# Optimization experiments

Hardware: AMD Instinct MI355X
Metric: run time of the kernel (lower is better)

The kernel has to match this reference:

```python
import jax, jax.numpy as jnp
import numpy as np

# DCNv2 (ModulatedDeformConvPack) config, matching init_kwargs
STRIDE, PAD, DIL = 1, 1, 1
DG = 8            # deformable_groups
KH = KW = 3
CIN, COUT = 64, 64
B, H, W = 2, 128, 128


def setup_inputs() -> dict:
    key = jax.random.key(0)
    k1, k2, k3, k4 = jax.random.split(key, 4)
    x = jax.random.normal(k1, (B, CIN, H, W), dtype=jnp.float32)
    # conv_offset: Conv2d(CIN, DG*3*KH*KW, 3, stride=1, pad=1). Zero-init in the
    # original; use small random weights so offsets/mask are non-trivial.
    conv_offset_w = jax.random.normal(k2, (DG * 3 * KH * KW, CIN, KH, KW), dtype=jnp.float32) * 0.01
    conv_offset_b = jax.random.normal(k3, (DG * 3 * KH * KW,), dtype=jnp.float32) * 0.01
    n = CIN * KH * KW
    stdv = 1.0 / np.sqrt(n)
    weight = jax.random.uniform(k4, (COUT, CIN, KH, KW), dtype=jnp.float32, minval=-stdv, maxval=stdv)
    bias = jnp.zeros((COUT,), dtype=jnp.float32)
    return {"x": x, "conv_offset_w": conv_offset_w, "conv_offset_b": conv_offset_b,
            "weight": weight, "bias": bias}


def _dcn_v2(x, conv_offset_w, conv_offset_b, weight, bias):
    Bn, Cin, Hh, Ww = x.shape
    Cout, _, kh, kw = weight.shape
    K = kh * kw
    cpg = Cin // DG  # channels per deformable group

    # offset/mask predictor conv (standard conv)
    out = jax.lax.conv_general_dilated(
        x, conv_offset_w, window_strides=(STRIDE, STRIDE),
        padding=[(PAD, PAD), (PAD, PAD)], rhs_dilation=(DIL, DIL),
        dimension_numbers=("NCHW", "OIHW", "NCHW")) + conv_offset_b[None, :, None, None]
    o1, o2, mask = jnp.split(out, 3, axis=1)
    offset = jnp.concatenate([o1, o2], axis=1)          # (B, 2*DG*K, Ho, Wo)
    Ho, Wo = offset.shape[2], offset.shape[3]
    # CUDA kernel reads offset channels as [dg, K, (y, x)]
    off = offset.reshape(Bn, DG, K, 2, Ho, Wo)
    off_y = off[:, :, :, 0]                              # (B, DG, K, Ho, Wo)
    off_x = off[:, :, :, 1]
    mask = jax.nn.sigmoid(mask).reshape(Bn, DG, K, Ho, Wo)

    ki = (jnp.arange(K) // kw).astype(x.dtype)           # tap row index
    kj = (jnp.arange(K) % kw).astype(x.dtype)            # tap col index
    base_y = jnp.arange(Ho, dtype=x.dtype) * STRIDE - PAD
    base_x = jnp.arange(Wo, dtype=x.dtype) * STRIDE - PAD
    py = off_y + base_y[None, None, None, :, None] + (ki * DIL)[None, None, :, None, None]
    px = off_x + base_x[None, None, None, None, :] + (kj * DIL)[None, None, :, None, None]

    y0 = jnp.floor(py)
    x0 = jnp.floor(px)
    ly = py - y0
    lx = px - x0
    y0i = y0.astype(jnp.int32)
    x0i = x0.astype(jnp.int32)

    xg = x.reshape(Bn, DG, cpg, Hh, Ww)
    bi = jnp.arange(Bn)[:, None, None, None, None]
    gi = jnp.arange(DG)[None, :, None, None, None]

    def gather(yi, xi):
        # zero padding outside the image (matches CUDA corner validity checks)
        valid = (yi >= 0) & (yi <= Hh - 1) & (xi >= 0) & (xi <= Ww - 1)
        yc = jnp.clip(yi, 0, Hh - 1)
        xc = jnp.clip(xi, 0, Ww - 1)
        v = xg[bi, gi, :, yc, xc]                        # (B, DG, K, Ho, Wo, cpg)
        return v * valid[..., None].astype(x.dtype)

    v00 = gather(y0i, x0i)
    v01 = gather(y0i, x0i + 1)
    v10 = gather(y0i + 1, x0i)
    v11 = gather(y0i + 1, x0i + 1)
    hy, hx = 1.0 - ly, 1.0 - lx
    val = ((hy * hx)[..., None] * v00 + (hy * lx)[..., None] * v01 +
           (ly * hx)[..., None] * v10 + (ly * lx)[..., None] * v11)

    col = val * mask[..., None]                          # modulated columns
    wr = weight.reshape(Cout, DG, cpg, K)
    y = jnp.einsum('bgkhwc,ogck->bohw', col, wr) + bias[None, :, None, None]
    return y


def reference(x, conv_offset_w, conv_offset_b, weight, bias):
    return _dcn_v2(x, conv_offset_w, conv_offset_b, weight, bias)
```

## Files before the change

### kernel.cpp

```cpp
#include <hip/hip_runtime.h>
#include <hip/hip_fp16.h>

constexpr int BB = 2;
constexpr int CINc = 64;
constexpr int HWc = 128 * 128;
constexpr int OCOFFc = 216;
constexpr int XP = 130;

constexpr size_t XT_BYTES  = (size_t)BB * 8 * XP * XP * 8 * 2;
constexpr size_t WB1_OFF   = XT_BYTES;
constexpr size_t WB1_BYTES = (size_t)9 * 8 * 256 * 8 * 2;
constexpr size_t WM_OFF    = WB1_OFF + WB1_BYTES;
constexpr size_t WM_BYTES  = (size_t)8 * 12 * 64 * 8 * 2;
constexpr size_t WS_NEEDED = WM_OFF + WM_BYTES;

typedef _Float16 f16x8 __attribute__((ext_vector_type(8)));
typedef float    f32x4 __attribute__((ext_vector_type(4)));

__global__ void prep_all(const float* __restrict__ x, const float* __restrict__ w_off,
                         const float* __restrict__ weight,
                         __half* __restrict__ xT, __half* __restrict__ wB1,
                         __half* __restrict__ wM) {
    int bid = blockIdx.x;
    if (bid < 1024) {
        int site = bid * 256 + threadIdx.x;
        int pix = site & (HWc - 1);
        int bdg = site >> 14;
        int dg = bdg & 7, b = bdg >> 3;
        int y = pix >> 7, xc = pix & 127;
        const float* xp = x + (size_t)(b * CINc + dg * 8) * HWc + pix;
        __half2 h0 = __halves2half2(__float2half(xp[0 * HWc]), __float2half(xp[1 * HWc]));
        __half2 h1 = __halves2half2(__float2half(xp[2 * HWc]), __float2half(xp[3 * HWc]));
        __half2 h2 = __halves2half2(__float2half(xp[4 * HWc]), __float2half(xp[5 * HWc]));
        __half2 h3 = __halves2half2(__float2half(xp[6 * HWc]), __float2half(xp[7 * HWc]));
        __half2* o = reinterpret_cast<__half2*>(
            xT + (((size_t)(b * 8 + dg) * XP + y + 1) * XP + xc + 1) * 8);
        o[0] = h0; o[1] = h1; o[2] = h2; o[3] = h3;
        return;
    }
    int idx = (bid - 1024) * 256 + threadIdx.x;
    if (idx < 9 * 8 * 256 * 8) {
        int ci = idx & 7;
        int oc = (idx >> 3) & 255;
        int c  = (idx >> 11) & 7;
        int tap = idx >> 14;
        float v = (oc < OCOFFc) ? w_off[oc * 576 + (c * 8 + ci) * 9 + tap] : 0.f;
        wB1[idx] = __float2half(v);
    } else if (idx < 9 * 8 * 256 * 8 + 8 * 12 * 64 * 8) {
        int j = idx - 9 * 8 * 256 * 8;
        int c = j & 7;
        int oc = (j >> 3) & 63;
        int tg = j >> 9;
        int tap = tg % 12;
        int dg = tg / 12;
        float v = (tap < 9) ? weight[oc * 576 + (dg * 8 + c) * 9 + tap] : 0.f;
        wM[j] = __float2half(v);
    } else {
        int j2 = idx - (9 * 8 * 256 * 8 + 8 * 12 * 64 * 8);
        if (j2 < 16 * 516) {
            int plane = j2 / 516;
            int p = j2 - plane * 516;
            int y, xx;
            if (p < 130)      { y = 0;           xx = p; }
            else if (p < 260) { y = 129;         xx = p - 130; }
            else if (p < 388) { y = 1 + p - 260; xx = 0; }
            else              { y = 1 + p - 388; xx = 129; }
            uint4 z = {0u, 0u, 0u, 0u};
            *reinterpret_cast<uint4*>(xT + (((size_t)plane * XP + y) * XP + xx) * 8) = z;
        }
    }
}

#define DCN_ISSUE(DG, G, W)                                                    \
  {                                                                            \
    const int dg_ = (DG);                                                      \
    const __half* xb_ = xT + (size_t)(b * 8 + dg_) * XP * XP * 8;              \
    _Pragma("unroll")                                                          \
    for (int s_ = 0; s_ < 3; ++s_) {                                           \
      const int kg_ = s_ * 4 + lh;                                             \
      if (kg_ < 9) {                                                           \
        const int r3_ = (dg_ * 9 + kg_) * 3;                                   \
        float oy_ = __half2float(offsb[r3_ * 132 + px]);                       \
        float ox_ = __half2float(offsb[(r3_ + 1) * 132 + px]);                 \
        float mk_ = __half2float(offsb[(r3_ + 2) * 132 + px]);                 \
        const int ki_ = kg_ / 3, kj_ = kg_ - ki_ * 3;                          \
        float sy_ = oy_ + (float)(gy - 1 + ki_);                               \
        float sx_ = ox_ + (float)(gx - 1 + kj_);                               \
        float y0f_ = floorf(sy_), x0f_ = floorf(sx_);                          \
        int iy0_ = (int)y0f_, ix0_ = (int)x0f_;                                \
        float ly_ = sy_ - y0f_, lx_ = sx_ - x0f_;                              \
        float hy_ = 1.f - ly_, hx_ = 1.f - lx_;                                \
        float vy0_ = ((unsigned)iy0_ < 128u) ? 1.f : 0.f;                      \
        float vy1_ = ((unsigned)(iy0_ + 1) < 128u) ? 1.f : 0.f;                \
        float vx0_ = ((unsigned)ix0_ < 128u) ? 1.f : 0.f;                      \
        float vx1_ = ((unsigned)(ix0_ + 1) < 128u) ? 1.f : 0.f;                \
        W[s_ * 4 + 0] = hy_ * hx_ * vy0_ * vx0_ * mk_;                         \
        W[s_ * 4 + 1] = hy_ * lx_ * vy0_ * vx1_ * mk_;                         \
        W[s_ * 4 + 2] = ly_ * hx_ * vy1_ * vx0_ * mk_;                         \
        W[s_ * 4 + 3] = ly_ * lx_ * vy1_ * vx1_ * mk_;                         \
        int y0c_ = min(max(iy0_, 0), 127), y1c_ = min(max(iy0_ + 1, 0), 127);  \
        int x0c_ = min(max(ix0_, 0), 127), x1c_ = min(max(ix0_ + 1, 0), 127);  \
        G[s_ * 4 + 0] = *reinterpret_cast<const float4*>(xb_ + ((size_t)(y0c_ + 1) * XP + x0c_ + 1) * 8); \
        G[s_ * 4 + 1] = *reinterpret_cast<const float4*>(xb_ + ((size_t)(y0c_ + 1) * XP + x1c_ + 1) * 8); \
        G[s_ * 4 + 2] = *reinterpret_cast<const float4*>(xb_ + ((size_t)(y1c_ + 1) * XP + x0c_ + 1) * 8); \
        G[s_ * 4 + 3] = *reinterpret_cast<const float4*>(xb_ + ((size_t)(y1c_ + 1) * XP + x1c_ + 1) * 8); \
      } else {                                                                 \
        const float4 z4_ = {0.f, 0.f, 0.f, 0.f};                               \
        W[s_ * 4 + 0] = 0.f; W[s_ * 4 + 1] = 0.f;                              \
        W[s_ * 4 + 2] = 0.f; W[s_ * 4 + 3] = 0.f;                              \
        G[s_ * 4 + 0] = z4_; G[s_ * 4 + 1] = z4_;                              \
        G[s_ * 4 + 2] = z4_; G[s_ * 4 + 3] = z4_;                              \
      }                                                                        \
    }                                                                          \
  }

#define DCN_CONSUME(DG, G, W)                                                  \
  {                                                                            \
    const int dg_ = (DG);                                                      \
    f16x8 bf_[12];                                                             \
    _Pragma("unroll")                                                          \
    for (int s_ = 0; s_ < 3; ++s_)                                             \
      _Pragma("unroll")                                                        \
      for (int n_ = 0; n_ < 4; ++n_)                                           \
        bf_[s_ * 4 + n_] = *reinterpret_cast<const f16x8*>(                    \
            wM + (size_t)((dg_ * 12 + s_ * 4 + lh) * 64 + n_ * 16 + l15) * 8); \
    f16x8 af_[3];                                                              \
    _Pragma("unroll")                                                          \
    for (int s_ = 0; s_ < 3; ++s_) {                                           \
      __half2 W00_ = __float2half2_rn(W[s_ * 4 + 0]);                          \
      __half2 W01_ = __float2half2_rn(W[s_ * 4 + 1]);                          \
      __half2 W10_ = __float2half2_rn(W[s_ * 4 + 2]);                          \
      __half2 W11_ = __float2half2_rn(W[s_ * 4 + 3]);                          \
      const __half2* a00_ = reinterpret_cast<const __half2*>(&G[s_ * 4 + 0]);  \
      const __half2* a01_ = reinterpret_cast<const __half2*>(&G[s_ * 4 + 1]);  \
      const __half2* a10_ = reinterpret_cast<const __half2*>(&G[s_ * 4 + 2]);  \
      const __half2* a11_ = reinterpret_cast<const __half2*>(&G[s_ * 4 + 3]);  \
      __align__(16) __half2 rr_[4];                                            \
      _Pragma("unroll")                                                        \
      for (int cc_ = 0; cc_ < 4; ++cc_)                                        \
        rr_[cc_] = __hfma2(a00_[cc_], W00_,                                    \
                   __hfma2(a01_[cc_], W01_,                                    \
                   __hfma2(a10_[cc_], W10_, __hmul2(a11_[cc_], W11_))));       \
      af_[s_] = *reinterpret_cast<const f16x8*>(rr_);                          \
    }                                                                          \
    _Pragma("unroll")                                                          \
    for (int s_ = 0; s_ < 3; ++s_)                                             \
      _Pragma("unroll")                                                        \
      for (int n_ = 0; n_ < 4; ++n_)                                           \
        acc2[n_] = __builtin_amdgcn_mfma_f32_16x16x32_f16(                     \
            af_[s_], bf_[s_ * 4 + n_], acc2[n_], 0, 0, 0);                     \
  }

__global__ __launch_bounds__(512, 2) void dcn_fused_k(
        const __half* __restrict__ xT, const __half* __restrict__ wB1,
        const float* __restrict__ cob, const __half* __restrict__ wM,
        const float* __restrict__ bias, float* __restrict__ out) {
    __shared__ __half xs[1440 * 8];
    __shared__ __half offsb[216 * 132];
    const int tid = threadIdx.x;
    const int fid = blockIdx.x + (blockIdx.y << 3) + (blockIdx.z << 7);
    const int vid = ((fid & 7) << 5) + (fid >> 3);
    const int bx = vid & 7;
    const int by = (vid >> 3) & 15;
    const int b  = vid >> 7;

    #pragma unroll
    for (int it = 0; it < 3; ++it) {
        int idx = tid + it * 512;
        if (idx < 1440) {
            int yl = idx / 144;
            int rem = idx - yl * 144;
            int cl = rem >> 3, sl = rem & 7;
            int dg = sl ^ (cl & 7);
            float4 v = *reinterpret_cast<const float4*>(
                xT + (((size_t)(b * 8 + dg) * XP + by * 8 + yl) * XP + bx * 16 + cl) * 8);
            *reinterpret_cast<float4*>(xs + idx * 8) = v;
        }
    }
    __syncthreads();

    const int lane = tid & 63;
    const int wid = tid >> 6;
    const int l15 = lane & 15, lh = lane >> 4;

    {
        const int wr = wid & 1;
        const int wc = wid >> 1;
        f32x4 acc[4][4];
        const f32x4 zero = {0.f, 0.f, 0.f, 0.f};
        #pragma unroll
        for (int ty = 0; ty < 4; ++ty)
            #pragma unroll
            for (int ot = 0; ot < 4; ++ot) acc[ty][ot] = zero;

        #pragma unroll 3
        for (int tap = 0; tap < 9; ++tap) {
            const int r = tap / 3, s = tap - r * 3;
            const int j = l15 + s;
            #pragma unroll
            for (int h = 0; h < 2; ++h) {
                const int c = h * 4 + lh;
                const int sl = c ^ (j & 7);
                f16x8 af[4], bf[4];
                #pragma unroll
                for (int ot = 0; ot < 4; ++ot) {
                    int oc = wc * 64 + ot * 16 + l15;
                    bf[ot] = *reinterpret_cast<const f16x8*>(
                        wB1 + (size_t)(((tap * 8 + c) * 256 + oc)) * 8);
                }
                #pragma unroll
                for (int ty = 0; ty < 4; ++ty) {
                    int row = wr * 4 + ty + r;
                    af[ty] = *reinterpret_cast<const f16x8*>(xs + (row * 18 + j) * 64 + sl * 8);
                }
                #pragma unroll
                for (int ty = 0; ty < 4; ++ty)
                    #pragma unroll
                    for (int ot = 0; ot < 4; ++ot)
                        acc[ty][ot] = __builtin_amdgcn_mfma_f32_16x16x32_f16(
                            af[ty], bf[ot], acc[ty][ot], 0, 0, 0);
            }
        }

        #pragma unroll
        for (int ot = 0; ot < 4; ++ot) {
            int oc = wc * 64 + ot * 16 + l15;
            if (oc < OCOFFc) {
                float bi = cob[oc];
                bool sig = (oc >= 144);
                int dg, k, comp;
                if (oc < 144) { dg = oc / 18; int rem = oc - dg * 18; k = rem >> 1; comp = rem & 1; }
                else          { int mm = oc - 144; dg = mm / 9; k = mm - dg * 9; comp = 2; }
                int r3 = (dg * 9 + k) * 3 + comp;
                #pragma unroll
                for (int ty = 0; ty < 4; ++ty) {
                    int px = (wr * 4 + ty) * 16 + lh * 4;
                    float v0 = acc[ty][ot][0] + bi, v1 = acc[ty][ot][1] + bi;
                    float v2 = acc[ty][ot][2] + bi, v3 = acc[ty][ot][3] + bi;
                    if (sig) {
                        v0 = 1.f / (1.f + __expf(-v0)); v1 = 1.f / (1.f + __expf(-v1));
                        v2 = 1.f / (1.f + __expf(-v2)); v3 = 1.f / (1.f + __expf(-v3));
                    }
                    __half2* d = reinterpret_cast<__half2*>(&offsb[r3 * 132 + px]);
                    d[0] = __halves2half2(__float2half(v0), __float2half(v1));
                    d[1] = __halves2half2(__float2half(v2), __float2half(v3));
                }
            }
        }
    }
    __syncthreads();

    const int px = wid * 16 + l15;
    const int gy = by * 8 + wid;
    const int gx = bx * 16 + l15;

    f32x4 acc2[4];
    const f32x4 zero2 = {0.f, 0.f, 0.f, 0.f};
    #pragma unroll
    for (int n = 0; n < 4; ++n) acc2[n] = zero2;

    float4 gA[12]; float wA[12];
    float4 gB[12]; float wB[12];

    DCN_ISSUE(0, gA, wA);
    #pragma unroll 1
    for (int d = 0; d < 8; d += 2) {
        DCN_ISSUE(d + 1, gB, wB);
        DCN_CONSUME(d, gA, wA);
        if (d + 2 < 8) DCN_ISSUE(d + 2, gA, wA);
        DCN_CONSUME(d + 1, gB, wB);
    }

    #pragma unroll
    for (int n = 0; n < 4; ++n) {
        int oc = n * 16 + l15;
        float bi = bias[oc];
        float4 v = make_float4(acc2[n][0] + bi, acc2[n][1] + bi,
                               acc2[n][2] + bi, acc2[n][3] + bi);
        *reinterpret_cast<float4*>(
            out + (size_t)(b * 64 + oc) * HWc + gy * 128 + bx * 16 + lh * 4) = v;
    }
}

extern "C" void kernel_launch(void* const* d_in, const int* in_sizes, int n_in,
                              void* d_out, int out_size, void* d_ws, size_t ws_size,
                              hipStream_t stream) {
    const float* x      = (const float*)d_in[0];
    const float* w_off  = (const float*)d_in[1];
    const float* cob    = (const float*)d_in[2];
    const float* weight = (const float*)d_in[3];
    const float* bias   = (const float*)d_in[4];
    float* out = (float*)d_out;
    if (ws_size < WS_NEEDED) return;

    char* ws = (char*)d_ws;
    __half* xT  = (__half*)ws;
    __half* wB1 = (__half*)(ws + WB1_OFF);
    __half* wM  = (__half*)(ws + WM_OFF);

    prep_all<<<1825, 256, 0, stream>>>(x, w_off, weight, xT, wB1, wM);
    dcn_fused_k<<<dim3(8, 16, 2), 512, 0, stream>>>(xT, wB1, cob, wM, bias, out);
}
```

Baseline: 39.36 us.

## Halve fused DCN tile to 8x8 pixels and split output channels across waves

Each block of the fused kernel now covers an 8x8 pixel tile instead of 8x16, which doubles the grid to 512 blocks and halves the shared-memory footprint for the input halo and offset buffer. The offset-conv MFMA tiling is remapped so each wave covers 32 pixels, and the deformable stage splits the 64 output channels between wave halves, with each wave handling 16 pixels and 32 channels. The goal is to raise occupancy and CU coverage on a small problem. The cost is that bilinear sampling and weight computation are now done twice per pixel (once per channel half), and the halo overhead per pixel is higher.

```diff
diff --git a/kernel.cpp b/kernel.cpp
--- a/kernel.cpp
+++ b/kernel.cpp
@@ -80,9 +80,9 @@
       const int kg_ = s_ * 4 + lh;                                             \
       if (kg_ < 9) {                                                           \
         const int r3_ = (dg_ * 9 + kg_) * 3;                                   \
-        float oy_ = __half2float(offsb[r3_ * 132 + px]);                       \
-        float ox_ = __half2float(offsb[(r3_ + 1) * 132 + px]);                 \
-        float mk_ = __half2float(offsb[(r3_ + 2) * 132 + px]);                 \
+        float oy_ = __half2float(offsb[r3_ * 66 + px]);                        \
+        float ox_ = __half2float(offsb[(r3_ + 1) * 66 + px]);                  \
+        float mk_ = __half2float(offsb[(r3_ + 2) * 66 + px]);                  \
         const int ki_ = kg_ / 3, kj_ = kg_ - ki_ * 3;                          \
         float sy_ = oy_ + (float)(gy - 1 + ki_);                               \
         float sx_ = ox_ + (float)(gx - 1 + kj_);                               \
@@ -117,13 +117,13 @@
 #define DCN_CONSUME(DG, G, W)                                                  \
   {                                                                            \
     const int dg_ = (DG);                                                      \
-    f16x8 bf_[12];                                                             \
+    f16x8 bf_[6];                                                              \
     _Pragma("unroll")                                                          \
     for (int s_ = 0; s_ < 3; ++s_)                                             \
       _Pragma("unroll")                                                        \
-      for (int n_ = 0; n_ < 4; ++n_)                                           \
-        bf_[s_ * 4 + n_] = *reinterpret_cast<const f16x8*>(                    \
-            wM + (size_t)((dg_ * 12 + s_ * 4 + lh) * 64 + n_ * 16 + l15) * 8); \
+      for (int n_ = 0; n_ < 2; ++n_)                                           \
+        bf_[s_ * 2 + n_] = *reinterpret_cast<const f16x8*>(                    \
+            wM + (size_t)((dg_ * 12 + s_ * 4 + lh) * 64 + nh * 32 + n_ * 16 + l15) * 8); \
     f16x8 af_[3];                                                              \
     _Pragma("unroll")                                                          \
     for (int s_ = 0; s_ < 3; ++s_) {                                           \
@@ -146,34 +146,34 @@
     _Pragma("unroll")                                                          \
     for (int s_ = 0; s_ < 3; ++s_)                                             \
       _Pragma("unroll")                                                        \
-      for (int n_ = 0; n_ < 4; ++n_)                                           \
+      for (int n_ = 0; n_ < 2; ++n_)                                           \
         acc2[n_] = __builtin_amdgcn_mfma_f32_16x16x32_f16(                     \
-            af_[s_], bf_[s_ * 4 + n_], acc2[n_], 0, 0, 0);                     \
+            af_[s_], bf_[s_ * 2 + n_], acc2[n_], 0, 0, 0);                     \
   }
 
 __global__ __launch_bounds__(512, 2) void dcn_fused_k(
         const __half* __restrict__ xT, const __half* __restrict__ wB1,
         const float* __restrict__ cob, const __half* __restrict__ wM,
         const float* __restrict__ bias, float* __restrict__ out) {
-    __shared__ __half xs[1440 * 8];
-    __shared__ __half offsb[216 * 132];
+    __shared__ __half xs[800 * 8];
+    __shared__ __half offsb[216 * 66];
     const int tid = threadIdx.x;
-    const int fid = blockIdx.x + (blockIdx.y << 3) + (blockIdx.z << 7);
-    const int vid = ((fid & 7) << 5) + (fid >> 3);
-    const int bx = vid & 7;
-    const int by = (vid >> 3) & 15;
-    const int b  = vid >> 7;
+    const int fid = blockIdx.x + (blockIdx.y << 4) + (blockIdx.z << 8);
+    const int vid = ((fid & 7) << 6) + (fid >> 3);
+    const int bx = vid & 15;
+    const int by = (vid >> 4) & 15;
+    const int b  = vid >> 8;
 
     #pragma unroll
-    for (int it = 0; it < 3; ++it) {
+    for (int it = 0; it < 2; ++it) {
         int idx = tid + it * 512;
-        if (idx < 1440) {
-            int yl = idx / 144;
-            int rem = idx - yl * 144;
+        if (idx < 800) {
+            int yl = idx / 80;
+            int rem = idx - yl * 80;
             int cl = rem >> 3, sl = rem & 7;
             int dg = sl ^ (cl & 7);
             float4 v = *reinterpret_cast<const float4*>(
-                xT + (((size_t)(b * 8 + dg) * XP + by * 8 + yl) * XP + bx * 16 + cl) * 8);
+                xT + (((size_t)(b * 8 + dg) * XP + by * 8 + yl) * XP + bx * 8 + cl) * 8);
             *reinterpret_cast<float4*>(xs + idx * 8) = v;
         }
     }
@@ -184,47 +184,47 @@
     const int l15 = lane & 15, lh = lane >> 4;
 
     {
-        const int wr = wid & 1;
-        const int wc = wid >> 1;
-        f32x4 acc[4][4];
+        const int wm = wid & 1;
+        const int wn = wid >> 1;
+        f32x4 acc[2][4];
         const f32x4 zero = {0.f, 0.f, 0.f, 0.f};
         #pragma unroll
-        for (int ty = 0; ty < 4; ++ty)
+        for (int f = 0; f < 2; ++f)
             #pragma unroll
-            for (int ot = 0; ot < 4; ++ot) acc[ty][ot] = zero;
+            for (int ot = 0; ot < 4; ++ot) acc[f][ot] = zero;
 
         #pragma unroll 3
         for (int tap = 0; tap < 9; ++tap) {
             const int r = tap / 3, s = tap - r * 3;
-            const int j = l15 + s;
+            const int j = (l15 & 7) + s;
             #pragma unroll
             for (int h = 0; h < 2; ++h) {
                 const int c = h * 4 + lh;
                 const int sl = c ^ (j & 7);
-                f16x8 af[4], bf[4];
+                f16x8 af[2], bf[4];
                 #pragma unroll
                 for (int ot = 0; ot < 4; ++ot) {
-                    int oc = wc * 64 + ot * 16 + l15;
+                    int oc = wn * 64 + ot * 16 + l15;
                     bf[ot] = *reinterpret_cast<const f16x8*>(
                         wB1 + (size_t)(((tap * 8 + c) * 256 + oc)) * 8);
                 }
                 #pragma unroll
-                for (int ty = 0; ty < 4; ++ty) {
-                    int row = wr * 4 + ty + r;
-                    af[ty] = *reinterpret_cast<const f16x8*>(xs + (row * 18 + j) * 64 + sl * 8);
+                for (int f = 0; f < 2; ++f) {
+                    int row = wm * 4 + f * 2 + (l15 >> 3) + r;
+                    af[f] = *reinterpret_cast<const f16x8*>(xs + (row * 10 + j) * 64 + sl * 8);
                 }
                 #pragma unroll
-                for (int ty = 0; ty < 4; ++ty)
+                for (int f = 0; f < 2; ++f)
                     #pragma unroll
                     for (int ot = 0; ot < 4; ++ot)
-                        acc[ty][ot] = __builtin_amdgcn_mfma_f32_16x16x32_f16(
-                            af[ty], bf[ot], acc[ty][ot], 0, 0, 0);
+                        acc[f][ot] = __builtin_amdgcn_mfma_f32_16x16x32_f16(
+                            af[f], bf[ot], acc[f][ot], 0, 0, 0);
             }
         }
 
         #pragma unroll
         for (int ot = 0; ot < 4; ++ot) {
-            int oc = wc * 64 + ot * 16 + l15;
+            int oc = wn * 64 + ot * 16 + l15;
             if (oc < OCOFFc) {
                 float bi = cob[oc];
                 bool sig = (oc >= 144);
@@ -233,15 +233,15 @@
                 else          { int mm = oc - 144; dg = mm / 9; k = mm - dg * 9; comp = 2; }
                 int r3 = (dg * 9 + k) * 3 + comp;
                 #pragma unroll
-                for (int ty = 0; ty < 4; ++ty) {
-                    int px = (wr * 4 + ty) * 16 + lh * 4;
-                    float v0 = acc[ty][ot][0] + bi, v1 = acc[ty][ot][1] + bi;
-                    float v2 = acc[ty][ot][2] + bi, v3 = acc[ty][ot][3] + bi;
+                for (int f = 0; f < 2; ++f) {
+                    int px = wm * 32 + f * 16 + lh * 4;
+                    float v0 = acc[f][ot][0] + bi, v1 = acc[f][ot][1] + bi;
+                    float v2 = acc[f][ot][2] + bi, v3 = acc[f][ot][3] + bi;
                     if (sig) {
                         v0 = 1.f / (1.f + __expf(-v0)); v1 = 1.f / (1.f + __expf(-v1));
                         v2 = 1.f / (1.f + __expf(-v2)); v3 = 1.f / (1.f + __expf(-v3));
                     }
-                    __half2* d = reinterpret_cast<__half2*>(&offsb[r3 * 132 + px]);
+                    __half2* d = reinterpret_cast<__half2*>(&offsb[r3 * 66 + px]);
                     d[0] = __halves2half2(__float2half(v0), __float2half(v1));
                     d[1] = __halves2half2(__float2half(v2), __float2half(v3));
                 }
@@ -250,14 +250,14 @@
     }
     __syncthreads();
 
-    const int px = wid * 16 + l15;
-    const int gy = by * 8 + wid;
-    const int gx = bx * 16 + l15;
-
-    f32x4 acc2[4];
+    const int m  = wid & 3;
+    const int nh = wid >> 2;
+    const int px = m * 16 + l15;
+    const int gy = by * 8 + (px >> 3), gx = bx * 8 + (px & 7);
+
+    f32x4 acc2[2];
     const f32x4 zero2 = {0.f, 0.f, 0.f, 0.f};
-    #pragma unroll
-    for (int n = 0; n < 4; ++n) acc2[n] = zero2;
+    acc2[0] = zero2; acc2[1] = zero2;
 
     float4 gA[12]; float wA[12];
     float4 gB[12]; float wB[12];
@@ -271,14 +271,16 @@
         DCN_CONSUME(d + 1, gB, wB);
     }
 
+    const int gyo = by * 8 + m * 2 + (lh >> 1);
+    const int gx0 = bx * 8 + (lh & 1) * 4;
     #pragma unroll
-    for (int n = 0; n < 4; ++n) {
-        int oc = n * 16 + l15;
+    for (int n = 0; n < 2; ++n) {
+        int oc = nh * 32 + n * 16 + l15;
         float bi = bias[oc];
         float4 v = make_float4(acc2[n][0] + bi, acc2[n][1] + bi,
                                acc2[n][2] + bi, acc2[n][3] + bi);
         *reinterpret_cast<float4*>(
-            out + (size_t)(b * 64 + oc) * HWc + gy * 128 + bx * 16 + lh * 4) = v;
+            out + (size_t)(b * 64 + oc) * HWc + gyo * 128 + gx0) = v;
     }
 }
 
@@ -299,5 +301,5 @@
     __half* wM  = (__half*)(ws + WM_OFF);
 
     prep_all<<<1825, 256, 0, stream>>>(x, w_off, weight, xT, wB1, wM);
-    dcn_fused_k<<<dim3(8, 16, 2), 512, 0, stream>>>(xT, wB1, cob, wM, bias, out);
+    dcn_fused_k<<<dim3(16, 16, 2), 512, 0, stream>>>(xT, wB1, cob, wM, bias, out);
 }
```

Result: slower. 49.65 us (+26.1%).

## Software-pipeline weight fragment loads and raise MFMA priority in fused DCN kernel

Applied to the files above, without the earlier changes.

Weight B-fragments for both the offset conv and the deformable MFMA stage are now prefetched one step ahead into double buffers, so global loads overlap the preceding MFMA batch. MFMA sections are wrapped in s_setprio to favour matrix issue, bilinear weights are packed as half2 to save registers, and the offset LDS row pitch shrinks from 132 to 130. Launch bounds drop from 2 to 1 block per CU, giving more registers for the extra buffers at the cost of occupancy.

```diff
diff --git a/kernel.cpp b/kernel.cpp
--- a/kernel.cpp
+++ b/kernel.cpp
@@ -71,6 +71,17 @@
     }
 }
 
+#define DCN_LOADBF(DG, BF)                                                     \
+  {                                                                            \
+    const int dgb_ = (DG);                                                     \
+    _Pragma("unroll")                                                          \
+    for (int s_ = 0; s_ < 3; ++s_)                                             \
+      _Pragma("unroll")                                                        \
+      for (int n_ = 0; n_ < 4; ++n_)                                           \
+        BF[s_ * 4 + n_] = *reinterpret_cast<const f16x8*>(                     \
+            wM + (size_t)((dgb_ * 12 + s_ * 4 + lh) * 64 + n_ * 16 + l15) * 8);\
+  }
+
 #define DCN_ISSUE(DG, G, W)                                                    \
   {                                                                            \
     const int dg_ = (DG);                                                      \
@@ -80,9 +91,9 @@
       const int kg_ = s_ * 4 + lh;                                             \
       if (kg_ < 9) {                                                           \
         const int r3_ = (dg_ * 9 + kg_) * 3;                                   \
-        float oy_ = __half2float(offsb[r3_ * 132 + px]);                       \
-        float ox_ = __half2float(offsb[(r3_ + 1) * 132 + px]);                 \
-        float mk_ = __half2float(offsb[(r3_ + 2) * 132 + px]);                 \
+        float oy_ = __half2float(offsb[r3_ * 130 + px]);                       \
+        float ox_ = __half2float(offsb[(r3_ + 1) * 130 + px]);                 \
+        float mk_ = __half2float(offsb[(r3_ + 2) * 130 + px]);                 \
         const int ki_ = kg_ / 3, kj_ = kg_ - ki_ * 3;                          \
         float sy_ = oy_ + (float)(gy - 1 + ki_);                               \
         float sx_ = ox_ + (float)(gx - 1 + kj_);                               \
@@ -94,10 +105,10 @@
         float vy1_ = ((unsigned)(iy0_ + 1) < 128u) ? 1.f : 0.f;                \
         float vx0_ = ((unsigned)ix0_ < 128u) ? 1.f : 0.f;                      \
         float vx1_ = ((unsigned)(ix0_ + 1) < 128u) ? 1.f : 0.f;                \
-        W[s_ * 4 + 0] = hy_ * hx_ * vy0_ * vx0_ * mk_;                         \
-        W[s_ * 4 + 1] = hy_ * lx_ * vy0_ * vx1_ * mk_;                         \
-        W[s_ * 4 + 2] = ly_ * hx_ * vy1_ * vx0_ * mk_;                         \
-        W[s_ * 4 + 3] = ly_ * lx_ * vy1_ * vx1_ * mk_;                         \
+        W[s_ * 2 + 0] = __floats2half2_rn(hy_ * hx_ * vy0_ * vx0_ * mk_,      \
+                                          hy_ * lx_ * vy0_ * vx1_ * mk_);      \
+        W[s_ * 2 + 1] = __floats2half2_rn(ly_ * hx_ * vy1_ * vx0_ * mk_,      \
+                                          ly_ * lx_ * vy1_ * vx1_ * mk_);      \
         int y0c_ = min(max(iy0_, 0), 127), y1c_ = min(max(iy0_ + 1, 0), 127);  \
         int x0c_ = min(max(ix0_, 0), 127), x1c_ = min(max(ix0_ + 1, 0), 127);  \
         G[s_ * 4 + 0] = *reinterpret_cast<const float4*>(xb_ + ((size_t)(y0c_ + 1) * XP + x0c_ + 1) * 8); \
@@ -106,31 +117,23 @@
         G[s_ * 4 + 3] = *reinterpret_cast<const float4*>(xb_ + ((size_t)(y1c_ + 1) * XP + x1c_ + 1) * 8); \
       } else {                                                                 \
         const float4 z4_ = {0.f, 0.f, 0.f, 0.f};                               \
-        W[s_ * 4 + 0] = 0.f; W[s_ * 4 + 1] = 0.f;                              \
-        W[s_ * 4 + 2] = 0.f; W[s_ * 4 + 3] = 0.f;                              \
+        W[s_ * 2 + 0] = __float2half2_rn(0.f);                                 \
+        W[s_ * 2 + 1] = __float2half2_rn(0.f);                                 \
         G[s_ * 4 + 0] = z4_; G[s_ * 4 + 1] = z4_;                              \
         G[s_ * 4 + 2] = z4_; G[s_ * 4 + 3] = z4_;                              \
       }                                                                        \
     }                                                                          \
   }
 
-#define DCN_CONSUME(DG, G, W)                                                  \
+#define DCN_CONSUME(DG, G, W, BF)                                              \
   {                                                                            \
-    const int dg_ = (DG);                                                      \
-    f16x8 bf_[12];                                                             \
-    _Pragma("unroll")                                                          \
-    for (int s_ = 0; s_ < 3; ++s_)                                             \
-      _Pragma("unroll")                                                        \
-      for (int n_ = 0; n_ < 4; ++n_)                                           \
-        bf_[s_ * 4 + n_] = *reinterpret_cast<const f16x8*>(                    \
-            wM + (size_t)((dg_ * 12 + s_ * 4 + lh) * 64 + n_ * 16 + l15) * 8); \
     f16x8 af_[3];                                                              \
     _Pragma("unroll")                                                          \
     for (int s_ = 0; s_ < 3; ++s_) {                                           \
-      __half2 W00_ = __float2half2_rn(W[s_ * 4 + 0]);                          \
-      __half2 W01_ = __float2half2_rn(W[s_ * 4 + 1]);                          \
-      __half2 W10_ = __float2half2_rn(W[s_ * 4 + 2]);                          \
-      __half2 W11_ = __float2half2_rn(W[s_ * 4 + 3]);                          \
+      __half2 W00_ = __half2half2(__low2half(W[s_ * 2 + 0]));                  \
+      __half2 W01_ = __half2half2(__high2half(W[s_ * 2 + 0]));                 \
+      __half2 W10_ = __half2half2(__low2half(W[s_ * 2 + 1]));                  \
+      __half2 W11_ = __half2half2(__high2half(W[s_ * 2 + 1]));                 \
       const __half2* a00_ = reinterpret_cast<const __half2*>(&G[s_ * 4 + 0]);  \
       const __half2* a01_ = reinterpret_cast<const __half2*>(&G[s_ * 4 + 1]);  \
       const __half2* a10_ = reinterpret_cast<const __half2*>(&G[s_ * 4 + 2]);  \
@@ -143,20 +146,22 @@
                    __hfma2(a10_[cc_], W10_, __hmul2(a11_[cc_], W11_))));       \
       af_[s_] = *reinterpret_cast<const f16x8*>(rr_);                          \
     }                                                                          \
+    __builtin_amdgcn_s_setprio(1);                                             \
     _Pragma("unroll")                                                          \
     for (int s_ = 0; s_ < 3; ++s_)                                             \
       _Pragma("unroll")                                                        \
       for (int n_ = 0; n_ < 4; ++n_)                                           \
         acc2[n_] = __builtin_amdgcn_mfma_f32_16x16x32_f16(                     \
-            af_[s_], bf_[s_ * 4 + n_], acc2[n_], 0, 0, 0);                     \
+            af_[s_], BF[s_ * 4 + n_], acc2[n_], 0, 0, 0);                      \
+    __builtin_amdgcn_s_setprio(0);                                             \
   }
 
-__global__ __launch_bounds__(512, 2) void dcn_fused_k(
+__global__ __launch_bounds__(512, 1) void dcn_fused_k(
         const __half* __restrict__ xT, const __half* __restrict__ wB1,
         const float* __restrict__ cob, const __half* __restrict__ wM,
         const float* __restrict__ bias, float* __restrict__ out) {
     __shared__ __half xs[1440 * 8];
-    __shared__ __half offsb[216 * 132];
+    __shared__ __half offsb[216 * 130];
     const int tid = threadIdx.x;
     const int fid = blockIdx.x + (blockIdx.y << 3) + (blockIdx.z << 7);
     const int vid = ((fid & 7) << 5) + (fid >> 3);
@@ -186,6 +191,7 @@
     {
         const int wr = wid & 1;
         const int wc = wid >> 1;
+        const int ocb = wc * 64 + l15;
         f32x4 acc[4][4];
         const f32x4 zero = {0.f, 0.f, 0.f, 0.f};
         #pragma unroll
@@ -193,32 +199,58 @@
             #pragma unroll
             for (int ot = 0; ot < 4; ++ot) acc[ty][ot] = zero;
 
-        #pragma unroll 3
+        f16x8 bfA[4], bfB[4];
+        #pragma unroll
+        for (int ot = 0; ot < 4; ++ot)
+            bfA[ot] = *reinterpret_cast<const f16x8*>(
+                wB1 + (size_t)(lh * 256 + ocb + ot * 16) * 8);
+
+        #pragma unroll 1
         for (int tap = 0; tap < 9; ++tap) {
             const int r = tap / 3, s = tap - r * 3;
             const int j = l15 + s;
             #pragma unroll
-            for (int h = 0; h < 2; ++h) {
-                const int c = h * 4 + lh;
-                const int sl = c ^ (j & 7);
-                f16x8 af[4], bf[4];
-                #pragma unroll
-                for (int ot = 0; ot < 4; ++ot) {
-                    int oc = wc * 64 + ot * 16 + l15;
-                    bf[ot] = *reinterpret_cast<const f16x8*>(
-                        wB1 + (size_t)(((tap * 8 + c) * 256 + oc)) * 8);
-                }
-                #pragma unroll
-                for (int ty = 0; ty < 4; ++ty) {
-                    int row = wr * 4 + ty + r;
-                    af[ty] = *reinterpret_cast<const f16x8*>(xs + (row * 18 + j) * 64 + sl * 8);
-                }
+            for (int ot = 0; ot < 4; ++ot)
+                bfB[ot] = *reinterpret_cast<const f16x8*>(
+                    wB1 + (size_t)((tap * 8 + 4 + lh) * 256 + ocb + ot * 16) * 8);
+            {
+                const int sl = lh ^ (j & 7);
+                f16x8 af[4];
+                #pragma unroll
+                for (int ty = 0; ty < 4; ++ty)
+                    af[ty] = *reinterpret_cast<const f16x8*>(
+                        xs + ((wr * 4 + ty + r) * 18 + j) * 64 + sl * 8);
+                __builtin_amdgcn_s_setprio(1);
                 #pragma unroll
                 for (int ty = 0; ty < 4; ++ty)
                     #pragma unroll
                     for (int ot = 0; ot < 4; ++ot)
                         acc[ty][ot] = __builtin_amdgcn_mfma_f32_16x16x32_f16(
-                            af[ty], bf[ot], acc[ty][ot], 0, 0, 0);
+                            af[ty], bfA[ot], acc[ty][ot], 0, 0, 0);
+                __builtin_amdgcn_s_setprio(0);
+            }
+            if (tap < 8) {
+                #pragma unroll
+                for (int ot = 0; ot < 4; ++ot)
+                    bfA[ot] = *reinterpret_cast<const f16x8*>(
+                        wB1 + (size_t)(((tap + 1) * 8 + lh) * 256 + ocb + ot * 16) * 8);
+            }
+            {
+                const int c = 4 + lh;
+                const int sl = c ^ (j & 7);
+                f16x8 af[4];
+                #pragma unroll
+                for (int ty = 0; ty < 4; ++ty)
+                    af[ty] = *reinterpret_cast<const f16x8*>(
+                        xs + ((wr * 4 + ty + r) * 18 + j) * 64 + sl * 8);
+                __builtin_amdgcn_s_setprio(1);
+                #pragma unroll
+                for (int ty = 0; ty < 4; ++ty)
+                    #pragma unroll
+                    for (int ot = 0; ot < 4; ++ot)
+                        acc[ty][ot] = __builtin_amdgcn_mfma_f32_16x16x32_f16(
+                            af[ty], bfB[ot], acc[ty][ot], 0, 0, 0);
+                __builtin_amdgcn_s_setprio(0);
             }
         }
 
@@ -241,7 +273,7 @@
                         v0 = 1.f / (1.f + __expf(-v0)); v1 = 1.f / (1.f + __expf(-v1));
                         v2 = 1.f / (1.f + __expf(-v2)); v3 = 1.f / (1.f + __expf(-v3));
                     }
-                    __half2* d = reinterpret_cast<__half2*>(&offsb[r3 * 132 + px]);
+                    __half2* d = reinterpret_cast<__half2*>(&offsb[r3 * 130 + px]);
                     d[0] = __halves2half2(__float2half(v0), __float2half(v1));
                     d[1] = __halves2half2(__float2half(v2), __float2half(v3));
                 }
@@ -259,16 +291,22 @@
     #pragma unroll
     for (int n = 0; n < 4; ++n) acc2[n] = zero2;
 
-    float4 gA[12]; float wA[12];
-    float4 gB[12]; float wB[12];
-
-    DCN_ISSUE(0, gA, wA);
+    float4 gX[12], gY[12];
+    __half2 wX[6], wY[6];
+    f16x8 bfX[12], bfY[12];
+
+    DCN_LOADBF(0, bfX);
+    DCN_ISSUE(0, gX, wX);
     #pragma unroll 1
     for (int d = 0; d < 8; d += 2) {
-        DCN_ISSUE(d + 1, gB, wB);
-        DCN_CONSUME(d, gA, wA);
-        if (d + 2 < 8) DCN_ISSUE(d + 2, gA, wA);
-        DCN_CONSUME(d + 1, gB, wB);
+        DCN_LOADBF(d + 1, bfY);
+        DCN_ISSUE(d + 1, gY, wY);
+        DCN_CONSUME(d, gX, wX, bfX);
+        if (d < 6) {
+            DCN_LOADBF(d + 2, bfX);
+            DCN_ISSUE(d + 2, gX, wX);
+        }
+        DCN_CONSUME(d + 1, gY, wY, bfY);
     }
 
     #pragma unroll
```

Result: slower. 58.64 us (+49.0%).

## Pipeline deformable sampling per tap-slice with fp16 weights and repacked offset layout

Applied to the files above, without the earlier changes.

Splits each deformable group's gather-and-MFMA work into three tap slices and double-buffers at slice granularity rather than per full group. Per-slice weight fragments are loaded alongside the gathers, and the bilinear weights are stored as packed half2. The shared offset/mask buffer is reorganized pixel-major so each thread fetches offset-y, offset-x and mask with one 8-byte load. The aim is lower register pressure and finer overlap of gather latency with MFMA, at the cost of scattered 2-byte shared stores in the offset epilogue and possible bank conflicts from the stride-36 layout.

```diff
diff --git a/kernel.cpp b/kernel.cpp
--- a/kernel.cpp
+++ b/kernel.cpp
@@ -71,18 +71,23 @@
     }
 }
 
-#define DCN_ISSUE(DG, G, W)                                                    \
+#define DCN_IC(D_, S_, BF, G, W, ACT)                                          \
   {                                                                            \
-    const int dg_ = (DG);                                                      \
-    const __half* xb_ = xT + (size_t)(b * 8 + dg_) * XP * XP * 8;              \
-    _Pragma("unroll")                                                          \
-    for (int s_ = 0; s_ < 3; ++s_) {                                           \
-      const int kg_ = s_ * 4 + lh;                                             \
-      if (kg_ < 9) {                                                           \
-        const int r3_ = (dg_ * 9 + kg_) * 3;                                   \
-        float oy_ = __half2float(offsb[r3_ * 132 + px]);                       \
-        float ox_ = __half2float(offsb[(r3_ + 1) * 132 + px]);                 \
-        float mk_ = __half2float(offsb[(r3_ + 2) * 132 + px]);                 \
+    const int dci_ = (D_);                                                     \
+    if (ACT) {                                                                 \
+      _Pragma("unroll")                                                        \
+      for (int n_ = 0; n_ < 4; ++n_)                                           \
+        BF[n_] = *reinterpret_cast<const f16x8*>(                              \
+            wM + (size_t)((dci_ * 12 + (S_) * 4 + lh) * 64 + n_ * 16 + l15) * 8); \
+      const int kg_ = (S_) * 4 + lh;                                           \
+      if ((S_) < 2 || lh == 0) {                                               \
+        uint2 ov_ = *reinterpret_cast<const uint2*>(                           \
+            offsb + ((size_t)(dci_ * 128 + px)) * 36 + kg_ * 4);               \
+        __half2 p0_ = *reinterpret_cast<const __half2*>(&ov_.x);               \
+        __half2 p1_ = *reinterpret_cast<const __half2*>(&ov_.y);               \
+        float oy_ = __half2float(__low2half(p0_));                             \
+        float ox_ = __half2float(__high2half(p0_));                            \
+        float mk_ = __half2float(__low2half(p1_));                             \
         const int ki_ = kg_ / 3, kj_ = kg_ - ki_ * 3;                          \
         float sy_ = oy_ + (float)(gy - 1 + ki_);                               \
         float sx_ = ox_ + (float)(gx - 1 + kj_);                               \
@@ -94,61 +99,52 @@
         float vy1_ = ((unsigned)(iy0_ + 1) < 128u) ? 1.f : 0.f;                \
         float vx0_ = ((unsigned)ix0_ < 128u) ? 1.f : 0.f;                      \
         float vx1_ = ((unsigned)(ix0_ + 1) < 128u) ? 1.f : 0.f;                \
-        W[s_ * 4 + 0] = hy_ * hx_ * vy0_ * vx0_ * mk_;                         \
-        W[s_ * 4 + 1] = hy_ * lx_ * vy0_ * vx1_ * mk_;                         \
-        W[s_ * 4 + 2] = ly_ * hx_ * vy1_ * vx0_ * mk_;                         \
-        W[s_ * 4 + 3] = ly_ * lx_ * vy1_ * vx1_ * mk_;                         \
+        W[0] = __floats2half2_rn(hy_ * hx_ * vy0_ * vx0_ * mk_,                \
+                                 hy_ * lx_ * vy0_ * vx1_ * mk_);               \
+        W[1] = __floats2half2_rn(ly_ * hx_ * vy1_ * vx0_ * mk_,                \
+                                 ly_ * lx_ * vy1_ * vx1_ * mk_);               \
         int y0c_ = min(max(iy0_, 0), 127), y1c_ = min(max(iy0_ + 1, 0), 127);  \
         int x0c_ = min(max(ix0_, 0), 127), x1c_ = min(max(ix0_ + 1, 0), 127);  \
-        G[s_ * 4 + 0] = *reinterpret_cast<const float4*>(xb_ + ((size_t)(y0c_ + 1) * XP + x0c_ + 1) * 8); \
-        G[s_ * 4 + 1] = *reinterpret_cast<const float4*>(xb_ + ((size_t)(y0c_ + 1) * XP + x1c_ + 1) * 8); \
-        G[s_ * 4 + 2] = *reinterpret_cast<const float4*>(xb_ + ((size_t)(y1c_ + 1) * XP + x0c_ + 1) * 8); \
-        G[s_ * 4 + 3] = *reinterpret_cast<const float4*>(xb_ + ((size_t)(y1c_ + 1) * XP + x1c_ + 1) * 8); \
+        const __half* xb_ = xT + (size_t)(b * 8 + dci_) * XP * XP * 8;         \
+        G[0] = *reinterpret_cast<const float4*>(xb_ + ((size_t)(y0c_ + 1) * XP + x0c_ + 1) * 8); \
+        G[1] = *reinterpret_cast<const float4*>(xb_ + ((size_t)(y0c_ + 1) * XP + x1c_ + 1) * 8); \
+        G[2] = *reinterpret_cast<const float4*>(xb_ + ((size_t)(y1c_ + 1) * XP + x0c_ + 1) * 8); \
+        G[3] = *reinterpret_cast<const float4*>(xb_ + ((size_t)(y1c_ + 1) * XP + x1c_ + 1) * 8); \
       } else {                                                                 \
         const float4 z4_ = {0.f, 0.f, 0.f, 0.f};                               \
-        W[s_ * 4 + 0] = 0.f; W[s_ * 4 + 1] = 0.f;                              \
-        W[s_ * 4 + 2] = 0.f; W[s_ * 4 + 3] = 0.f;                              \
-        G[s_ * 4 + 0] = z4_; G[s_ * 4 + 1] = z4_;                              \
-        G[s_ * 4 + 2] = z4_; G[s_ * 4 + 3] = z4_;                              \
+        W[0] = __float2half2_rn(0.f); W[1] = __float2half2_rn(0.f);            \
+        G[0] = z4_; G[1] = z4_; G[2] = z4_; G[3] = z4_;                        \
       }                                                                        \
+    } else {                                                                   \
+      const float4 z4_ = {0.f, 0.f, 0.f, 0.f};                                 \
+      const f16x8 zf_ = {0, 0, 0, 0, 0, 0, 0, 0};                              \
+      W[0] = __float2half2_rn(0.f); W[1] = __float2half2_rn(0.f);              \
+      G[0] = z4_; G[1] = z4_; G[2] = z4_; G[3] = z4_;                          \
+      BF[0] = zf_; BF[1] = zf_; BF[2] = zf_; BF[3] = zf_;                      \
     }                                                                          \
   }
 
-#define DCN_CONSUME(DG, G, W)                                                  \
+#define DCN_CC(BF, G, W)                                                       \
   {                                                                            \
-    const int dg_ = (DG);                                                      \
-    f16x8 bf_[12];                                                             \
+    __half2 W00_ = __half2half2(__low2half(W[0]));                             \
+    __half2 W01_ = __half2half2(__high2half(W[0]));                            \
+    __half2 W10_ = __half2half2(__low2half(W[1]));                             \
+    __half2 W11_ = __half2half2(__high2half(W[1]));                            \
+    const __half2* a00_ = reinterpret_cast<const __half2*>(&G[0]);             \
+    const __half2* a01_ = reinterpret_cast<const __half2*>(&G[1]);             \
+    const __half2* a10_ = reinterpret_cast<const __half2*>(&G[2]);             \
+    const __half2* a11_ = reinterpret_cast<const __half2*>(&G[3]);             \
+    __align__(16) __half2 rr_[4];                                              \
     _Pragma("unroll")                                                          \
-    for (int s_ = 0; s_ < 3; ++s_)                                             \
-      _Pragma("unroll")                                                        \
-      for (int n_ = 0; n_ < 4; ++n_)                                           \
-        bf_[s_ * 4 + n_] = *reinterpret_cast<const f16x8*>(                    \
-            wM + (size_t)((dg_ * 12 + s_ * 4 + lh) * 64 + n_ * 16 + l15) * 8); \
-    f16x8 af_[3];                                                              \
+    for (int cc_ = 0; cc_ < 4; ++cc_)                                          \
+      rr_[cc_] = __hfma2(a00_[cc_], W00_,                                      \
+                 __hfma2(a01_[cc_], W01_,                                      \
+                 __hfma2(a10_[cc_], W10_, __hmul2(a11_[cc_], W11_))));         \
+    f16x8 af_ = *reinterpret_cast<const f16x8*>(rr_);                          \
     _Pragma("unroll")                                                          \
-    for (int s_ = 0; s_ < 3; ++s_) {                                           \
-      __half2 W00_ = __float2half2_rn(W[s_ * 4 + 0]);                          \
-      __half2 W01_ = __float2half2_rn(W[s_ * 4 + 1]);                          \
-      __half2 W10_ = __float2half2_rn(W[s_ * 4 + 2]);                          \
-      __half2 W11_ = __float2half2_rn(W[s_ * 4 + 3]);                          \
-      const __half2* a00_ = reinterpret_cast<const __half2*>(&G[s_ * 4 + 0]);  \
-      const __half2* a01_ = reinterpret_cast<const __half2*>(&G[s_ * 4 + 1]);  \
-      const __half2* a10_ = reinterpret_cast<const __half2*>(&G[s_ * 4 + 2]);  \
-      const __half2* a11_ = reinterpret_cast<const __half2*>(&G[s_ * 4 + 3]);  \
-      __align__(16) __half2 rr_[4];                                            \
-      _Pragma("unroll")                                                        \
-      for (int cc_ = 0; cc_ < 4; ++cc_)                                        \
-        rr_[cc_] = __hfma2(a00_[cc_], W00_,                                    \
-                   __hfma2(a01_[cc_], W01_,                                    \
-                   __hfma2(a10_[cc_], W10_, __hmul2(a11_[cc_], W11_))));       \
-      af_[s_] = *reinterpret_cast<const f16x8*>(rr_);                          \
-    }                                                                          \
-    _Pragma("unroll")                                                          \
-    for (int s_ = 0; s_ < 3; ++s_)                                             \
-      _Pragma("unroll")                                                        \
-      for (int n_ = 0; n_ < 4; ++n_)                                           \
-        acc2[n_] = __builtin_amdgcn_mfma_f32_16x16x32_f16(                     \
-            af_[s_], bf_[s_ * 4 + n_], acc2[n_], 0, 0, 0);                     \
+    for (int n_ = 0; n_ < 4; ++n_)                                             \
+      acc2[n_] = __builtin_amdgcn_mfma_f32_16x16x32_f16(                       \
+          af_, BF[n_], acc2[n_], 0, 0, 0);                                     \
   }
 
 __global__ __launch_bounds__(512, 2) void dcn_fused_k(
@@ -156,7 +152,7 @@
         const float* __restrict__ cob, const __half* __restrict__ wM,
         const float* __restrict__ bias, float* __restrict__ out) {
     __shared__ __half xs[1440 * 8];
-    __shared__ __half offsb[216 * 132];
+    __shared__ __half offsb[8 * 128 * 36];
     const int tid = threadIdx.x;
     const int fid = blockIdx.x + (blockIdx.y << 3) + (blockIdx.z << 7);
     const int vid = ((fid & 7) << 5) + (fid >> 3);
@@ -231,19 +227,20 @@
                 int dg, k, comp;
                 if (oc < 144) { dg = oc / 18; int rem = oc - dg * 18; k = rem >> 1; comp = rem & 1; }
                 else          { int mm = oc - 144; dg = mm / 9; k = mm - dg * 9; comp = 2; }
-                int r3 = (dg * 9 + k) * 3 + comp;
                 #pragma unroll
                 for (int ty = 0; ty < 4; ++ty) {
-                    int px = (wr * 4 + ty) * 16 + lh * 4;
+                    int pxw = (wr * 4 + ty) * 16 + lh * 4;
                     float v0 = acc[ty][ot][0] + bi, v1 = acc[ty][ot][1] + bi;
                     float v2 = acc[ty][ot][2] + bi, v3 = acc[ty][ot][3] + bi;
                     if (sig) {
                         v0 = 1.f / (1.f + __expf(-v0)); v1 = 1.f / (1.f + __expf(-v1));
                         v2 = 1.f / (1.f + __expf(-v2)); v3 = 1.f / (1.f + __expf(-v3));
                     }
-                    __half2* d = reinterpret_cast<__half2*>(&offsb[r3 * 132 + px]);
-                    d[0] = __halves2half2(__float2half(v0), __float2half(v1));
-                    d[1] = __halves2half2(__float2half(v2), __float2half(v3));
+                    size_t base = (size_t)(dg * 128) * 36 + k * 4 + comp;
+                    offsb[base + (size_t)(pxw + 0) * 36] = __float2half(v0);
+                    offsb[base + (size_t)(pxw + 1) * 36] = __float2half(v1);
+                    offsb[base + (size_t)(pxw + 2) * 36] = __float2half(v2);
+                    offsb[base + (size_t)(pxw + 3) * 36] = __float2half(v3);
                 }
             }
         }
@@ -259,16 +256,20 @@
     #pragma unroll
     for (int n = 0; n < 4; ++n) acc2[n] = zero2;
 
-    float4 gA[12]; float wA[12];
-    float4 gB[12]; float wB[12];
-
-    DCN_ISSUE(0, gA, wA);
+    f16x8 bfX[4], bfY[4];
+    float4 gX[4], gY[4];
+    __half2 wX[2], wY[2];
+
+    DCN_IC(0, 0, bfX, gX, wX, true);
     #pragma unroll 1
-    for (int d = 0; d < 8; d += 2) {
-        DCN_ISSUE(d + 1, gB, wB);
-        DCN_CONSUME(d, gA, wA);
-        if (d + 2 < 8) DCN_ISSUE(d + 2, gA, wA);
-        DCN_CONSUME(d + 1, gB, wB);
+    for (int dp = 0; dp < 4; ++dp) {
+        const int d0 = dp * 2;
+        DCN_IC(d0,     1, bfY, gY, wY, true);     DCN_CC(bfX, gX, wX);
+        DCN_IC(d0,     2, bfX, gX, wX, true);     DCN_CC(bfY, gY, wY);
+        DCN_IC(d0 + 1, 0, bfY, gY, wY, true);     DCN_CC(bfX, gX, wX);
+        DCN_IC(d0 + 1, 1, bfX, gX, wX, true);     DCN_CC(bfY, gY, wY);
+        DCN_IC(d0 + 1, 2, bfY, gY, wY, true);     DCN_CC(bfX, gX, wX);
+        DCN_IC(d0 + 2, 0, bfX, gX, wX, dp < 3);   DCN_CC(bfY, gY, wY);
     }
 
     #pragma unroll
```

Result: faster. 38.06 us (-3.3%).
